# Optimization experiments

Measured on AMD Instinct MI355X. Metric: run time of the kernel, lower is better.

## Reference

```python
import jax, jax.numpy as jnp
import numpy as np

N_NODES = 50000
N_EDGES = 800000
D_IN = 128
D_OUT = 128


def setup_inputs() -> dict:
    key = jax.random.key(0)
    k = jax.random.split(key, 6)
    x = jax.random.normal(k[0], (N_NODES, D_IN), dtype=jnp.float32)
    weight = jax.random.normal(k[1], (D_IN, D_OUT), dtype=jnp.float32) * (1.0 / np.sqrt(D_IN))
    bias = jax.random.normal(k[2], (D_OUT,), dtype=jnp.float32)
    src = jax.random.randint(k[3], (N_EDGES,), 0, N_NODES, dtype=jnp.int32)
    dst = jax.random.randint(k[4], (N_EDGES,), 0, N_NODES, dtype=jnp.int32)
    edge_vals = jax.random.uniform(k[5], (N_EDGES,), dtype=jnp.float32)
    return {"x": x, "weight": weight, "bias": bias, "src": src, "dst": dst, "edge_vals": edge_vals}


def reference(x, weight, bias, src, dst, edge_vals):
    # support = x @ W  (dense projection), [N, D_OUT]
    support = jnp.matmul(x, weight)
    # spmm: out[d] = sum_{e: dst[e]==d} edge_vals[e] * support[src[e]]
    msgs = support[src] * edge_vals[:, None]  # [E, D_OUT]
    out = jax.ops.segment_sum(msgs, dst, num_segments=x.shape[0])
    return out + bias
```

## Files before the change

### kernel.cpp

```cpp
#include <hip/hip_runtime.h>
#include <hip/hip_bf16.h>

#define D 128
#define BKT 32
#define CAP 768
#define SC_EPB 4096
#define NBMAX 1600
#define CPAD 4

typedef __attribute__((ext_vector_type(8))) short bf16x8;
typedef __attribute__((ext_vector_type(4))) float f32x4;

__device__ __forceinline__ unsigned short f2bf(float f) {
  union { float f; unsigned u; } c; c.f = f;
  unsigned u = c.u + 0x7FFFu + ((c.u >> 16) & 1u);
  return (unsigned short)(u >> 16);
}
__device__ __forceinline__ float bf_lo(unsigned u) {
  union { unsigned u; float f; } c; c.u = u << 16; return c.f;
}
__device__ __forceinline__ float bf_hi(unsigned u) {
  union { unsigned u; float f; } c; c.u = u & 0xFFFF0000u; return c.f;
}

#define EV_Q 2047.0f
#define EV_IQ (1.0f / 2047.0f)

__global__ __launch_bounds__(256) void setup(
    const float* __restrict__ w, unsigned short* __restrict__ wT,
    int* __restrict__ bcur, int nb) {
  const int idx = blockIdx.x * 256 + threadIdx.x;
  if (idx < D * D) {
    const int k = idx >> 7, n = idx & 127;
    wT[n * D + k] = f2bf(w[idx]);
  }
  if (idx < nb) bcur[idx] = 0;
}

__global__ __launch_bounds__(512) void fused_scatter_gemm(
    const float* __restrict__ x, const unsigned short* __restrict__ wT,
    unsigned short* __restrict__ supb, int n_nodes,
    const int* __restrict__ src, const int* __restrict__ dst,
    const float* __restrict__ ev, int* __restrict__ bcur,
    unsigned* __restrict__ staged, int n_edges, int nb, int scat_blocks) {
  __shared__ char smem[64 * 136 * 2];
  const int t = threadIdx.x;

  if ((int)blockIdx.x >= scat_blocks) {
    unsigned short* xs = (unsigned short*)smem;
    const int row0 = ((int)blockIdx.x - scat_blocks) * 64;

    for (int f = t; f < 64 * 32; f += 512) {
      const int r = f >> 5, c4 = f & 31;
      const int gr = row0 + r;
      float4 v = make_float4(0.f, 0.f, 0.f, 0.f);
      if (gr < n_nodes) v = ((const float4*)(x + (size_t)gr * D))[c4];
      ushort4 b;
      b.x = f2bf(v.x); b.y = f2bf(v.y); b.z = f2bf(v.z); b.w = f2bf(v.w);
      *(ushort4*)(&xs[r * 136 + c4 * 4]) = b;
    }
    __syncthreads();

    const int w = t >> 6;
    const int rg = w & 3;
    const int ch = w >> 2;
    const int lane = t & 63;
    const int l15 = lane & 15;
    const int quad = lane >> 4;

    f32x4 acc[4];
#pragma unroll
    for (int q = 0; q < 4; q++) acc[q] = (f32x4){0.f, 0.f, 0.f, 0.f};

#pragma unroll
    for (int k0 = 0; k0 < D; k0 += 32) {
      const bf16x8 a =
          *(const bf16x8*)(&xs[(rg * 16 + l15) * 136 + k0 + quad * 8]);
      const unsigned short* wp =
          wT + (size_t)(ch * 64 + l15) * D + k0 + quad * 8;
#pragma unroll
      for (int q = 0; q < 4; q++) {
        const bf16x8 b = *(const bf16x8*)(wp + (size_t)q * 16 * D);
        acc[q] = __builtin_amdgcn_mfma_f32_16x16x32_bf16(a, b, acc[q], 0, 0, 0);
      }
    }

#pragma unroll
    for (int q = 0; q < 4; q++) {
      const int col = ch * 64 + q * 16 + l15;
#pragma unroll
      for (int r = 0; r < 4; r++) {
        const int row = row0 + rg * 16 + quad * 4 + r;
        if (row < n_nodes) supb[(size_t)row * D + col] = f2bf(acc[q][r]);
      }
    }
  } else {
    int* hist = (int*)smem;
    int* cur = hist + NBMAX;
    const int base = (int)blockIdx.x * SC_EPB;
    const int cnt = min(SC_EPB, n_edges - base);

    for (int i = t; i < nb; i += 512) hist[i] = 0;
    __syncthreads();
    for (int j = t; j < cnt; j += 512) atomicAdd(&hist[dst[base + j] >> 5], 1);
    __syncthreads();
    for (int i = t; i < nb; i += 512) {
      const int h = hist[i];
      cur[i] = h ? atomicAdd(&bcur[i], h) : 0;
    }
    __syncthreads();
    for (int j = t; j < cnt; j += 512) {
      const int e = base + j;
      const int d = dst[e];
      const int b = d >> 5;
      const int p = atomicAdd(&cur[b], 1);
      if (p < CAP) {
        const unsigned evq = (unsigned)__float2int_rn(ev[e] * EV_Q);
        staged[(size_t)b * CAP + p] =
            ((unsigned)src[e] << 16) | ((unsigned)(d & 31) << 11) | evq;
      }
    }
  }
}

__global__ __launch_bounds__(512) void bucket_reduce(
    const unsigned short* __restrict__ supb, const unsigned* __restrict__ staged,
    const int* __restrict__ bcnt, const float* __restrict__ bias,
    float* __restrict__ out, int n_nodes) {
  __shared__ unsigned rec[CAP];
  __shared__ unsigned ordered[CAP];
  __shared__ int hist[BKT];
  __shared__ int segbase[BKT];
  __shared__ int cur[BKT];
  __shared__ float comb[BKT][D + CPAD];

  const int t = threadIdx.x;
  const int b = blockIdx.x;
  const int lo = b << 5;
  const int cnt = min(bcnt[b], CAP);
  const unsigned* st = staged + (size_t)b * CAP;

  if (t < BKT) hist[t] = 0;
  __syncthreads();
  for (int j = t; j < cnt; j += 512) {
    const unsigned p = st[j];
    rec[j] = p;
    atomicAdd(&hist[(p >> 11) & 31], 1);
  }
  __syncthreads();
  if (t < BKT) {
    const int h = hist[t];
    int incl = h;
#pragma unroll
    for (int ofs = 1; ofs < BKT; ofs <<= 1) {
      const int v = __shfl_up(incl, ofs, 64);
      if (t >= ofs) incl += v;
    }
    segbase[t] = incl - h;
    cur[t] = incl - h;
  }
  __syncthreads();
  for (int j = t; j < cnt; j += 512) {
    const unsigned p = rec[j];
    const int pos = atomicAdd(&cur[(p >> 11) & 31], 1);
    ordered[pos] = p;
  }
  __syncthreads();

  const int n = t >> 4;
  const int h = (t >> 3) & 1;
  const int p8 = t & 7;
  const int beg = segbase[n];
  const int end = beg + hist[n];

  float a[16];
#pragma unroll
  for (int k = 0; k < 16; k++) a[k] = 0.f;

#define PROC1(pr, ra, rb)                                               \
  {                                                                     \
    const float v_ = (float)((pr) & 2047u) * EV_IQ;                     \
    a[0] += v_ * bf_lo((ra).x);  a[1] += v_ * bf_hi((ra).x);            \
    a[2] += v_ * bf_lo((ra).y);  a[3] += v_ * bf_hi((ra).y);            \
    a[4] += v_ * bf_lo((ra).z);  a[5] += v_ * bf_hi((ra).z);            \
    a[6] += v_ * bf_lo((ra).w);  a[7] += v_ * bf_hi((ra).w);            \
    a[8] += v_ * bf_lo((rb).x);  a[9] += v_ * bf_hi((rb).x);            \
    a[10] += v_ * bf_lo((rb).y); a[11] += v_ * bf_hi((rb).y);           \
    a[12] += v_ * bf_lo((rb).z); a[13] += v_ * bf_hi((rb).z);           \
    a[14] += v_ * bf_lo((rb).w); a[15] += v_ * bf_hi((rb).w);           \
  }

  int j = beg + h;
  for (; j + 2 < end; j += 4) {
    const unsigned pr0 = ordered[j];
    const unsigned pr1 = ordered[j + 2];
    const uint4* rp0 = (const uint4*)(supb + (size_t)(pr0 >> 16) * D);
    const uint4* rp1 = (const uint4*)(supb + (size_t)(pr1 >> 16) * D);
    const uint4 r0a = rp0[p8 * 2];
    const uint4 r0b = rp0[p8 * 2 + 1];
    const uint4 r1a = rp1[p8 * 2];
    const uint4 r1b = rp1[p8 * 2 + 1];
    PROC1(pr0, r0a, r0b);
    PROC1(pr1, r1a, r1b);
  }
  for (; j < end; j += 2) {
    const unsigned pr0 = ordered[j];
    const uint4* rp0 = (const uint4*)(supb + (size_t)(pr0 >> 16) * D);
    const uint4 r0a = rp0[p8 * 2];
    const uint4 r0b = rp0[p8 * 2 + 1];
    PROC1(pr0, r0a, r0b);
  }
#undef PROC1

  if (h == 1) {
#pragma unroll
    for (int q = 0; q < 4; q++)
      *(float4*)&comb[n][p8 * 16 + q * 4] =
          make_float4(a[q * 4], a[q * 4 + 1], a[q * 4 + 2], a[q * 4 + 3]);
  }
  __syncthreads();

  const int node = lo + n;
  if (h == 0 && node < n_nodes) {
#pragma unroll
    for (int q = 0; q < 4; q++) {
      const float4 cv = *(const float4*)&comb[n][p8 * 16 + q * 4];
      const float4 bv = ((const float4*)bias)[p8 * 4 + q];
      float4* op = (float4*)out + (size_t)node * 32 + p8 * 4 + q;
      *op = make_float4(a[q * 4] + cv.x + bv.x,
                        a[q * 4 + 1] + cv.y + bv.y,
                        a[q * 4 + 2] + cv.z + bv.z,
                        a[q * 4 + 3] + cv.w + bv.w);
    }
  }
}

extern "C" void kernel_launch(void* const* d_in, const int* in_sizes, int n_in,
                              void* d_out, int out_size, void* d_ws, size_t ws_size,
                              hipStream_t stream) {
  const float* x    = (const float*)d_in[0];
  const float* w    = (const float*)d_in[1];
  const float* bias = (const float*)d_in[2];
  const int*   src  = (const int*)d_in[3];
  const int*   dst  = (const int*)d_in[4];
  const float* ev   = (const float*)d_in[5];
  float* out = (float*)d_out;

  const int n_nodes = in_sizes[0] / D;
  const int n_edges = in_sizes[3];
  const int nb = (n_nodes + BKT - 1) / BKT;

  unsigned short* supb = (unsigned short*)d_ws;
  unsigned short* wT = supb + (size_t)n_nodes * D;
  int* bcur = (int*)(wT + D * D);
  unsigned* staged = (unsigned*)(bcur + NBMAX);

  setup<<<64, 256, 0, stream>>>(w, wT, bcur, nb);

  const int scat_blocks = (n_edges + SC_EPB - 1) / SC_EPB;
  const int gemm_blocks = (n_nodes + 63) / 64;
  fused_scatter_gemm<<<scat_blocks + gemm_blocks, 512, 0, stream>>>(
      x, wT, supb, n_nodes, src, dst, ev, bcur, staged, n_edges, nb,
      scat_blocks);

  bucket_reduce<<<nb, 512, 0, stream>>>(supb, staged, bcur, bias, out, n_nodes);
}
```

Baseline: 148.5 us.

## Load GEMM A fragments directly from global into registers, 128-row tiles

The GEMM part of the fused kernel no longer stages the x tile in shared memory. Each wave loads its 16 rows of x straight into bf16 MFMA fragments and computes all 128 output columns, so each block now covers 128 rows. This removes the LDS staging pass and its barrier and halves the GEMM block count. In exchange each wave makes twice as many global reads of W and uses more accumulator registers, and the shared array shrinks to what the scatter histogram needs, which may raise occupancy.

```diff
diff --git a/kernel.cpp b/kernel.cpp
--- a/kernel.cpp
+++ b/kernel.cpp
@@ -43,59 +43,60 @@
     const int* __restrict__ src, const int* __restrict__ dst,
     const float* __restrict__ ev, int* __restrict__ bcur,
     unsigned* __restrict__ staged, int n_edges, int nb, int scat_blocks) {
-  __shared__ char smem[64 * 136 * 2];
+  __shared__ int smem_i[2 * NBMAX];
   const int t = threadIdx.x;
 
   if ((int)blockIdx.x >= scat_blocks) {
-    unsigned short* xs = (unsigned short*)smem;
-    const int row0 = ((int)blockIdx.x - scat_blocks) * 64;
-
-    for (int f = t; f < 64 * 32; f += 512) {
-      const int r = f >> 5, c4 = f & 31;
-      const int gr = row0 + r;
-      float4 v = make_float4(0.f, 0.f, 0.f, 0.f);
-      if (gr < n_nodes) v = ((const float4*)(x + (size_t)gr * D))[c4];
-      ushort4 b;
-      b.x = f2bf(v.x); b.y = f2bf(v.y); b.z = f2bf(v.z); b.w = f2bf(v.w);
-      *(ushort4*)(&xs[r * 136 + c4 * 4]) = b;
-    }
-    __syncthreads();
-
+    const int gb = (int)blockIdx.x - scat_blocks;
     const int w = t >> 6;
-    const int rg = w & 3;
-    const int ch = w >> 2;
     const int lane = t & 63;
     const int l15 = lane & 15;
     const int quad = lane >> 4;
-
-    f32x4 acc[4];
-#pragma unroll
-    for (int q = 0; q < 4; q++) acc[q] = (f32x4){0.f, 0.f, 0.f, 0.f};
-
-#pragma unroll
-    for (int k0 = 0; k0 < D; k0 += 32) {
-      const bf16x8 a =
-          *(const bf16x8*)(&xs[(rg * 16 + l15) * 136 + k0 + quad * 8]);
-      const unsigned short* wp =
-          wT + (size_t)(ch * 64 + l15) * D + k0 + quad * 8;
-#pragma unroll
-      for (int q = 0; q < 4; q++) {
+    const int row0 = gb * 128;
+
+    const int arow = row0 + w * 16 + l15;
+    const int rowc = min(arow, n_nodes - 1);
+    const float* xr = x + (size_t)rowc * D;
+
+    bf16x8 af[4];
+#pragma unroll
+    for (int ks = 0; ks < 4; ks++) {
+      const float4 v0 = ((const float4*)xr)[ks * 8 + quad * 2];
+      const float4 v1 = ((const float4*)xr)[ks * 8 + quad * 2 + 1];
+      bf16x8 a;
+      a[0] = (short)f2bf(v0.x); a[1] = (short)f2bf(v0.y);
+      a[2] = (short)f2bf(v0.z); a[3] = (short)f2bf(v0.w);
+      a[4] = (short)f2bf(v1.x); a[5] = (short)f2bf(v1.y);
+      a[6] = (short)f2bf(v1.z); a[7] = (short)f2bf(v1.w);
+      af[ks] = a;
+    }
+
+    f32x4 acc[8];
+#pragma unroll
+    for (int q = 0; q < 8; q++) acc[q] = (f32x4){0.f, 0.f, 0.f, 0.f};
+
+#pragma unroll
+    for (int ks = 0; ks < 4; ks++) {
+      const unsigned short* wp = wT + (size_t)l15 * D + ks * 32 + quad * 8;
+#pragma unroll
+      for (int q = 0; q < 8; q++) {
         const bf16x8 b = *(const bf16x8*)(wp + (size_t)q * 16 * D);
-        acc[q] = __builtin_amdgcn_mfma_f32_16x16x32_bf16(a, b, acc[q], 0, 0, 0);
+        acc[q] = __builtin_amdgcn_mfma_f32_16x16x32_bf16(af[ks], b, acc[q],
+                                                         0, 0, 0);
       }
     }
 
 #pragma unroll
-    for (int q = 0; q < 4; q++) {
-      const int col = ch * 64 + q * 16 + l15;
+    for (int q = 0; q < 8; q++) {
+      const int col = q * 16 + l15;
 #pragma unroll
       for (int r = 0; r < 4; r++) {
-        const int row = row0 + rg * 16 + quad * 4 + r;
+        const int row = row0 + w * 16 + quad * 4 + r;
         if (row < n_nodes) supb[(size_t)row * D + col] = f2bf(acc[q][r]);
       }
     }
   } else {
-    int* hist = (int*)smem;
+    int* hist = smem_i;
     int* cur = hist + NBMAX;
     const int base = (int)blockIdx.x * SC_EPB;
     const int cnt = min(SC_EPB, n_edges - base);
@@ -258,7 +259,7 @@
   setup<<<64, 256, 0, stream>>>(w, wT, bcur, nb);
 
   const int scat_blocks = (n_edges + SC_EPB - 1) / SC_EPB;
-  const int gemm_blocks = (n_nodes + 63) / 64;
+  const int gemm_blocks = (n_nodes + 127) / 128;
   fused_scatter_gemm<<<scat_blocks + gemm_blocks, 512, 0, stream>>>(
       x, wT, supb, n_nodes, src, dst, ev, bcur, staged, n_edges, nb,
       scat_blocks);
```

Measured after the change: 150.4 us. Within noise of the previous version (+1.3%).

## Reorder to aggregate-then-project and fuse GEMM into bucket reduce

Applied to the files above, without the earlier changes.

Reassociates the computation so edges gather bf16-converted input rows and the dense projection runs on each bucket's aggregated 32-row tile inside the reduce kernel using MFMA. The first kernel now only converts x to bf16 alongside the edge scatter. This removes the separate GEMM pass and the write/read of the projected support array's dependency on the GEMM, but adds per-block weight loads, extra LDS, another sync, less coalesced output stores, and an extra bf16 rounding of aggregates.

```diff
diff --git a/kernel.cpp b/kernel.cpp
--- a/kernel.cpp
+++ b/kernel.cpp
@@ -7,6 +7,7 @@
 #define SC_EPB 4096
 #define NBMAX 1600
 #define CPAD 4
+#define XPAD 8
 
 typedef __attribute__((ext_vector_type(8))) short bf16x8;
 typedef __attribute__((ext_vector_type(4))) float f32x4;
@@ -37,65 +38,27 @@
   if (idx < nb) bcur[idx] = 0;
 }
 
-__global__ __launch_bounds__(512) void fused_scatter_gemm(
-    const float* __restrict__ x, const unsigned short* __restrict__ wT,
-    unsigned short* __restrict__ supb, int n_nodes,
+__global__ __launch_bounds__(512) void fused_scatter_convert(
+    const float* __restrict__ x, unsigned short* __restrict__ xb, int n_nodes,
     const int* __restrict__ src, const int* __restrict__ dst,
     const float* __restrict__ ev, int* __restrict__ bcur,
-    unsigned* __restrict__ staged, int n_edges, int nb, int scat_blocks) {
-  __shared__ char smem[64 * 136 * 2];
+    unsigned* __restrict__ staged, int n_edges, int nb, int scat_blocks,
+    int total_blocks) {
+  __shared__ int smem_i[2 * NBMAX];
   const int t = threadIdx.x;
 
   if ((int)blockIdx.x >= scat_blocks) {
-    unsigned short* xs = (unsigned short*)smem;
-    const int row0 = ((int)blockIdx.x - scat_blocks) * 64;
-
-    for (int f = t; f < 64 * 32; f += 512) {
-      const int r = f >> 5, c4 = f & 31;
-      const int gr = row0 + r;
-      float4 v = make_float4(0.f, 0.f, 0.f, 0.f);
-      if (gr < n_nodes) v = ((const float4*)(x + (size_t)gr * D))[c4];
+    const int nthr = (total_blocks - scat_blocks) * 512;
+    const int tid = ((int)blockIdx.x - scat_blocks) * 512 + t;
+    const int n4 = n_nodes * (D / 4);
+    for (int i = tid; i < n4; i += nthr) {
+      const float4 v = ((const float4*)x)[i];
       ushort4 b;
       b.x = f2bf(v.x); b.y = f2bf(v.y); b.z = f2bf(v.z); b.w = f2bf(v.w);
-      *(ushort4*)(&xs[r * 136 + c4 * 4]) = b;
-    }
-    __syncthreads();
-
-    const int w = t >> 6;
-    const int rg = w & 3;
-    const int ch = w >> 2;
-    const int lane = t & 63;
-    const int l15 = lane & 15;
-    const int quad = lane >> 4;
-
-    f32x4 acc[4];
-#pragma unroll
-    for (int q = 0; q < 4; q++) acc[q] = (f32x4){0.f, 0.f, 0.f, 0.f};
-
-#pragma unroll
-    for (int k0 = 0; k0 < D; k0 += 32) {
-      const bf16x8 a =
-          *(const bf16x8*)(&xs[(rg * 16 + l15) * 136 + k0 + quad * 8]);
-      const unsigned short* wp =
-          wT + (size_t)(ch * 64 + l15) * D + k0 + quad * 8;
-#pragma unroll
-      for (int q = 0; q < 4; q++) {
-        const bf16x8 b = *(const bf16x8*)(wp + (size_t)q * 16 * D);
-        acc[q] = __builtin_amdgcn_mfma_f32_16x16x32_bf16(a, b, acc[q], 0, 0, 0);
-      }
-    }
-
-#pragma unroll
-    for (int q = 0; q < 4; q++) {
-      const int col = ch * 64 + q * 16 + l15;
-#pragma unroll
-      for (int r = 0; r < 4; r++) {
-        const int row = row0 + rg * 16 + quad * 4 + r;
-        if (row < n_nodes) supb[(size_t)row * D + col] = f2bf(acc[q][r]);
-      }
+      ((ushort4*)xb)[i] = b;
     }
   } else {
-    int* hist = (int*)smem;
+    int* hist = smem_i;
     int* cur = hist + NBMAX;
     const int base = (int)blockIdx.x * SC_EPB;
     const int cnt = min(SC_EPB, n_edges - base);
@@ -123,16 +86,17 @@
   }
 }
 
-__global__ __launch_bounds__(512) void bucket_reduce(
-    const unsigned short* __restrict__ supb, const unsigned* __restrict__ staged,
-    const int* __restrict__ bcnt, const float* __restrict__ bias,
-    float* __restrict__ out, int n_nodes) {
+__global__ __launch_bounds__(512) void bucket_reduce_gemm(
+    const unsigned short* __restrict__ xb, const unsigned* __restrict__ staged,
+    const int* __restrict__ bcnt, const unsigned short* __restrict__ wT,
+    const float* __restrict__ bias, float* __restrict__ out, int n_nodes) {
   __shared__ unsigned rec[CAP];
   __shared__ unsigned ordered[CAP];
   __shared__ int hist[BKT];
   __shared__ int segbase[BKT];
   __shared__ int cur[BKT];
   __shared__ float comb[BKT][D + CPAD];
+  __shared__ unsigned short aggb[BKT][D + XPAD];
 
   const int t = threadIdx.x;
   const int b = blockIdx.x;
@@ -194,8 +158,8 @@
   for (; j + 2 < end; j += 4) {
     const unsigned pr0 = ordered[j];
     const unsigned pr1 = ordered[j + 2];
-    const uint4* rp0 = (const uint4*)(supb + (size_t)(pr0 >> 16) * D);
-    const uint4* rp1 = (const uint4*)(supb + (size_t)(pr1 >> 16) * D);
+    const uint4* rp0 = (const uint4*)(xb + (size_t)(pr0 >> 16) * D);
+    const uint4* rp1 = (const uint4*)(xb + (size_t)(pr1 >> 16) * D);
     const uint4 r0a = rp0[p8 * 2];
     const uint4 r0b = rp0[p8 * 2 + 1];
     const uint4 r1a = rp1[p8 * 2];
@@ -205,7 +169,7 @@
   }
   for (; j < end; j += 2) {
     const unsigned pr0 = ordered[j];
-    const uint4* rp0 = (const uint4*)(supb + (size_t)(pr0 >> 16) * D);
+    const uint4* rp0 = (const uint4*)(xb + (size_t)(pr0 >> 16) * D);
     const uint4 r0a = rp0[p8 * 2];
     const uint4 r0b = rp0[p8 * 2 + 1];
     PROC1(pr0, r0a, r0b);
@@ -219,18 +183,53 @@
           make_float4(a[q * 4], a[q * 4 + 1], a[q * 4 + 2], a[q * 4 + 3]);
   }
   __syncthreads();
-
-  const int node = lo + n;
-  if (h == 0 && node < n_nodes) {
+  if (h == 0) {
 #pragma unroll
     for (int q = 0; q < 4; q++) {
       const float4 cv = *(const float4*)&comb[n][p8 * 16 + q * 4];
-      const float4 bv = ((const float4*)bias)[p8 * 4 + q];
-      float4* op = (float4*)out + (size_t)node * 32 + p8 * 4 + q;
-      *op = make_float4(a[q * 4] + cv.x + bv.x,
-                        a[q * 4 + 1] + cv.y + bv.y,
-                        a[q * 4 + 2] + cv.z + bv.z,
-                        a[q * 4 + 3] + cv.w + bv.w);
+      ushort4 bb;
+      bb.x = f2bf(a[q * 4] + cv.x);
+      bb.y = f2bf(a[q * 4 + 1] + cv.y);
+      bb.z = f2bf(a[q * 4 + 2] + cv.z);
+      bb.w = f2bf(a[q * 4 + 3] + cv.w);
+      *(ushort4*)&aggb[n][p8 * 16 + q * 4] = bb;
+    }
+  }
+  __syncthreads();
+
+  const int wv = t >> 6;
+  const int rg = wv & 1;
+  const int cg = wv >> 1;
+  const int lane = t & 63;
+  const int l15 = lane & 15;
+  const int quad = lane >> 4;
+
+  f32x4 acc[2];
+  acc[0] = (f32x4){0.f, 0.f, 0.f, 0.f};
+  acc[1] = (f32x4){0.f, 0.f, 0.f, 0.f};
+
+#pragma unroll
+  for (int ks = 0; ks < 4; ks++) {
+    const bf16x8 av =
+        *(const bf16x8*)(&aggb[rg * 16 + l15][ks * 32 + quad * 8]);
+    const unsigned short* wp =
+        wT + (size_t)(cg * 32 + l15) * D + ks * 32 + quad * 8;
+#pragma unroll
+    for (int q = 0; q < 2; q++) {
+      const bf16x8 bv = *(const bf16x8*)(wp + (size_t)q * 16 * D);
+      acc[q] = __builtin_amdgcn_mfma_f32_16x16x32_bf16(av, bv, acc[q], 0, 0, 0);
+    }
+  }
+
+#pragma unroll
+  for (int q = 0; q < 2; q++) {
+    const int col = cg * 32 + q * 16 + l15;
+    const float bv = bias[col];
+#pragma unroll
+    for (int r = 0; r < 4; r++) {
+      const int row = rg * 16 + quad * 4 + r;
+      const int node = lo + row;
+      if (node < n_nodes) out[(size_t)node * D + col] = acc[q][r] + bv;
     }
   }
 }
@@ -250,18 +249,19 @@
   const int n_edges = in_sizes[3];
   const int nb = (n_nodes + BKT - 1) / BKT;
 
-  unsigned short* supb = (unsigned short*)d_ws;
-  unsigned short* wT = supb + (size_t)n_nodes * D;
+  unsigned short* xb = (unsigned short*)d_ws;
+  unsigned short* wT = xb + (size_t)n_nodes * D;
   int* bcur = (int*)(wT + D * D);
   unsigned* staged = (unsigned*)(bcur + NBMAX);
 
   setup<<<64, 256, 0, stream>>>(w, wT, bcur, nb);
 
   const int scat_blocks = (n_edges + SC_EPB - 1) / SC_EPB;
-  const int gemm_blocks = (n_nodes + 63) / 64;
-  fused_scatter_gemm<<<scat_blocks + gemm_blocks, 512, 0, stream>>>(
-      x, wT, supb, n_nodes, src, dst, ev, bcur, staged, n_edges, nb,
-      scat_blocks);
-
-  bucket_reduce<<<nb, 512, 0, stream>>>(supb, staged, bcur, bias, out, n_nodes);
-}
+  const int conv_blocks = 196;
+  fused_scatter_convert<<<scat_blocks + conv_blocks, 512, 0, stream>>>(
+      x, xb, n_nodes, src, dst, ev, bcur, staged, n_edges, nb,
+      scat_blocks, scat_blocks + conv_blocks);
+
+  bucket_reduce_gemm<<<nb, 512, 0, stream>>>(xb, staged, bcur, wT, bias, out,
+                                             n_nodes);
+}
```

After: 147.4 us. Within noise of the previous version (-0.7%).
